# Optimization experiments

Hardware: AMD Instinct MI355X
Metric: run time of the kernel (lower is better)

The kernel has to match this reference:

```python
import jax, jax.numpy as jnp
import numpy as np

N_NODES = 20000
N_EDGES = 640000
IN_CH = 128
HID = 128
NUM_GRAPHS = 64


def setup_inputs() -> dict:
    key = jax.random.key(0)
    ks = jax.random.split(key, 16)
    s_in = 1.0 / np.sqrt(IN_CH)
    s_h = 1.0 / np.sqrt(HID)
    return {
        "x": jax.random.normal(ks[0], (N_NODES, IN_CH), jnp.float32),
        "edge_index": jax.random.randint(ks[1], (2, N_EDGES), 0, N_NODES, jnp.int64),
        "batch": jnp.sort(jax.random.randint(ks[2], (N_NODES,), 0, NUM_GRAPHS, jnp.int64)),
        "W1a": jax.random.normal(ks[3], (IN_CH, HID), jnp.float32) * s_in,
        "b1a": jnp.zeros((HID,), jnp.float32),
        "W1b": jax.random.normal(ks[4], (HID, HID), jnp.float32) * s_h,
        "b1b": jnp.zeros((HID,), jnp.float32),
        "W2a": jax.random.normal(ks[5], (HID, HID), jnp.float32) * s_h,
        "b2a": jnp.zeros((HID,), jnp.float32),
        "W2b": jax.random.normal(ks[6], (HID, HID), jnp.float32) * s_h,
        "b2b": jnp.zeros((HID,), jnp.float32),
        "fc_w": jax.random.normal(ks[7], (HID, 1), jnp.float32) * s_h,
        "fc_b": jnp.zeros((1,), jnp.float32),
    }


def _gin_conv(x, edge_index, Wa, ba, Wb, bb):
    # PyG GINConv (eps=0, sum aggregation): MLP(x + scatter_add(x[src] -> dst))
    src, dst = edge_index[0], edge_index[1]
    agg = jax.ops.segment_sum(x[src], dst, num_segments=x.shape[0])
    h = x + agg
    h = jax.nn.relu(h @ Wa + ba)
    return h @ Wb + bb


def reference(x, edge_index, batch, W1a, b1a, W1b, b1b, W2a, b2a, W2b, b2b, fc_w, fc_b):
    h = jax.nn.relu(_gin_conv(x, edge_index, W1a, b1a, W1b, b1b))
    # dropout: inference mode -> identity
    h = jax.nn.relu(_gin_conv(h, edge_index, W2a, b2a, W2b, b2b))
    # global_mean_pool over graph ids
    sums = jax.ops.segment_sum(h, batch, num_segments=NUM_GRAPHS)
    counts = jax.ops.segment_sum(jnp.ones((h.shape[0],), h.dtype), batch, num_segments=NUM_GRAPHS)
    pooled = sums / jnp.maximum(counts, 1.0)[:, None]
    return pooled @ fc_w + fc_b
```

## Files before the change

### kernel.cpp

```cpp
#include <hip/hip_runtime.h>

#define NN 20000
#define NE 640000
#define CH 128
#define NG 64
#define CAP 96
#define CSTR 16

typedef unsigned short u16;
typedef unsigned char u8;
typedef __attribute__((ext_vector_type(8))) short short8;
typedef __attribute__((ext_vector_type(4))) float floatx4;
typedef __attribute__((ext_vector_type(2))) float floatx2;

__device__ __forceinline__ u16 f2b(float f) {
    unsigned int u = __float_as_uint(f);
    u += 0x7fff + ((u >> 16) & 1);
    return (u16)(u >> 16);
}
__device__ __forceinline__ u8 f2q(float f) {
    return (u8)(__builtin_amdgcn_cvt_pk_fp8_f32(f, f, 0, false) & 0xff);
}
__device__ __forceinline__ void acc16(uint4 q, floatx2* a) {
    a[0] += __builtin_amdgcn_cvt_pk_f32_fp8(q.x, false);
    a[1] += __builtin_amdgcn_cvt_pk_f32_fp8(q.x, true);
    a[2] += __builtin_amdgcn_cvt_pk_f32_fp8(q.y, false);
    a[3] += __builtin_amdgcn_cvt_pk_f32_fp8(q.y, true);
    a[4] += __builtin_amdgcn_cvt_pk_f32_fp8(q.z, false);
    a[5] += __builtin_amdgcn_cvt_pk_f32_fp8(q.z, true);
    a[6] += __builtin_amdgcn_cvt_pk_f32_fp8(q.w, false);
    a[7] += __builtin_amdgcn_cvt_pk_f32_fp8(q.w, true);
}
__device__ __forceinline__ void round32(const u8* __restrict__ in, const int* __restrict__ ssrc,
                                        int base, int slot, int boff, floatx2* a) {
    int4 si = *(const int4*)&ssrc[base + slot * 4];
    uint4 q0 = *(const uint4*)(in + (size_t)si.x * CH + boff);
    uint4 q1 = *(const uint4*)(in + (size_t)si.y * CH + boff);
    uint4 q2 = *(const uint4*)(in + (size_t)si.z * CH + boff);
    uint4 q3 = *(const uint4*)(in + (size_t)si.w * CH + boff);
    acc16(q0, a); acc16(q1, a); acc16(q2, a); acc16(q3, a);
}
__device__ __forceinline__ void tail32(const u8* __restrict__ in, const int* __restrict__ ssrc,
                                       int base, int e, int slot, int boff, floatx2* a) {
    int i0 = base + slot * 4;
    int4 si = *(const int4*)&ssrc[i0];
    bool ok0 = i0 + 0 < e, ok1 = i0 + 1 < e, ok2 = i0 + 2 < e, ok3 = i0 + 3 < e;
    int s0 = ok0 ? si.x : 0, s1 = ok1 ? si.y : 0, s2 = ok2 ? si.z : 0, s3 = ok3 ? si.w : 0;
    uint4 q0 = *(const uint4*)(in + (size_t)s0 * CH + boff);
    uint4 q1 = *(const uint4*)(in + (size_t)s1 * CH + boff);
    uint4 q2 = *(const uint4*)(in + (size_t)s2 * CH + boff);
    uint4 q3 = *(const uint4*)(in + (size_t)s3 * CH + boff);
    if (!ok0) q0 = make_uint4(0, 0, 0, 0);
    if (!ok1) q1 = make_uint4(0, 0, 0, 0);
    if (!ok2) q2 = make_uint4(0, 0, 0, 0);
    if (!ok3) q3 = make_uint4(0, 0, 0, 0);
    acc16(q0, a); acc16(q1, a); acc16(q2, a); acc16(q3, a);
}

__global__ __launch_bounds__(256) void prep(const float* __restrict__ x, u8* __restrict__ xq,
                                            const float* __restrict__ W1a, const float* __restrict__ W1b,
                                            const float* __restrict__ W2a, const float* __restrict__ W2b,
                                            u16* __restrict__ wt, float* __restrict__ gsum,
                                            const int* __restrict__ ei,
                                            int* __restrict__ cnt, int* __restrict__ ssrc) {
    int b = blockIdx.x;
    if (b < 2500) {
        int idx = (b * 256 + threadIdx.x) * 4;
        float4 v = *(const float4*)(x + idx);
        int pk = __builtin_amdgcn_cvt_pk_fp8_f32(v.x, v.y, 0, false);
        pk = __builtin_amdgcn_cvt_pk_fp8_f32(v.z, v.w, pk, true);
        *(unsigned int*)(xq + idx) = (unsigned int)pk;
    } else if (b < 2756) {
        int wi = b - 2500;
        int m = wi >> 6;
        int r = (wi & 63) * 256 + threadIdx.x;
        int j = r & 7, l16 = (r >> 3) & 15, quad = (r >> 7) & 3;
        int kc = (r >> 9) & 3, ct = (r >> 11) & 7;
        int n = ct * 16 + l16, k = kc * 32 + quad * 8 + j;
        const float* W = (m == 0) ? W1a : (m == 1) ? W1b : (m == 2) ? W2a : W2b;
        wt[m * 16384 + r] = f2b(W[k * 128 + n]);
    } else if (b < 2788) {
        gsum[(b - 2756) * 256 + threadIdx.x] = 0.f;
    } else {
        int e = (b - 2788) * 256 + threadIdx.x;
        int dst = ei[NE + e];
        int src = ei[e];
        int pos = atomicAdd(&cnt[dst * CSTR], 1);
        if (pos < CAP) ssrc[dst * CAP + pos] = src;
    }
}

template <int DO_POOL>
__global__ __launch_bounds__(512) void layer(const u8* __restrict__ in,
                                             const int* __restrict__ cnt, const int* __restrict__ ssrc,
                                             const u16* __restrict__ wtA, const u16* __restrict__ wtB,
                                             const float* __restrict__ biasA, const float* __restrict__ biasB,
                                             u8* __restrict__ outq,
                                             const int* __restrict__ batch, float* __restrict__ gsum) {
    __shared__ u16 A[16 * 136];
    __shared__ u16 H[16 * 136];
    int t = threadIdx.x, wave = t >> 6, lane = t & 63;
    int quad = lane >> 4, l16 = lane & 15;
    int nb = blockIdx.x * 16;

    int gg[4], glo = 0, ghi = 0;
    if (DO_POOL) {
        glo = batch[nb]; ghi = batch[nb + 15];
        #pragma unroll
        for (int r = 0; r < 4; ++r)
            gg[r] = batch[nb + quad * 4 + r];
    }

    int slot = lane >> 3, cg = lane & 7;
    int boff = cg * 16;
    {
        int n0 = nb + 2 * wave;
        int n1 = n0 + 1;
        int deg0 = cnt[n0 * CSTR]; if (deg0 > CAP) deg0 = CAP;
        int deg1 = cnt[n1 * CSTR]; if (deg1 > CAP) deg1 = CAP;
        floatx2 a0[8], a1[8];
        #pragma unroll
        for (int j = 0; j < 8; ++j) { a0[j] = (floatx2)(0.f); a1[j] = (floatx2)(0.f); }
        if (slot == 0) {
            uint4 q0 = *(const uint4*)(in + (size_t)n0 * CH + boff);
            uint4 q1 = *(const uint4*)(in + (size_t)n1 * CH + boff);
            acc16(q0, a0); acc16(q1, a1);
        }
        int b0 = n0 * CAP, e0 = b0 + deg0;
        int b1 = n1 * CAP, e1 = b1 + deg1;
        while ((b0 + 32 <= e0) | (b1 + 32 <= e1)) {
            if (b0 + 32 <= e0) { round32(in, ssrc, b0, slot, boff, a0); b0 += 32; }
            if (b1 + 32 <= e1) { round32(in, ssrc, b1, slot, boff, a1); b1 += 32; }
        }
        if (b0 < e0) tail32(in, ssrc, b0, e0, slot, boff, a0);
        if (b1 < e1) tail32(in, ssrc, b1, e1, slot, boff, a1);

        float f0[16], f1[16];
        #pragma unroll
        for (int j = 0; j < 8; ++j) {
            f0[2 * j] = a0[j][0]; f0[2 * j + 1] = a0[j][1];
            f1[2 * j] = a1[j][0]; f1[2 * j + 1] = a1[j][1];
        }
        #pragma unroll
        for (int j = 0; j < 16; ++j) {
            f0[j] += __shfl_xor(f0[j], 8);
            f0[j] += __shfl_xor(f0[j], 16);
            f0[j] += __shfl_xor(f0[j], 32);
            f1[j] += __shfl_xor(f1[j], 8);
            f1[j] += __shfl_xor(f1[j], 16);
            f1[j] += __shfl_xor(f1[j], 32);
        }
        if (slot == 0) {
            short8 o0a, o0b, o1a, o1b;
            #pragma unroll
            for (int j = 0; j < 8; ++j) {
                o0a[j] = (short)f2b(f0[j]);     o0b[j] = (short)f2b(f0[8 + j]);
                o1a[j] = (short)f2b(f1[j]);     o1b[j] = (short)f2b(f1[8 + j]);
            }
            *(short8*)&A[(2 * wave) * 136 + boff] = o0a;
            *(short8*)&A[(2 * wave) * 136 + boff + 8] = o0b;
            *(short8*)&A[(2 * wave + 1) * 136 + boff] = o1a;
            *(short8*)&A[(2 * wave + 1) * 136 + boff + 8] = o1b;
        }
    }
    __syncthreads();

    short8 af[4];
    #pragma unroll
    for (int kc = 0; kc < 4; ++kc)
        af[kc] = *(const short8*)&A[l16 * 136 + kc * 32 + quad * 8];

    {
        int ct = wave;
        floatx4 a0 = (floatx4)(0.f);
        #pragma unroll
        for (int kc = 0; kc < 4; ++kc) {
            short8 bf = *(const short8*)(wtA + (((ct * 4 + kc) * 4 + quad) * 16 + l16) * 8);
            a0 = __builtin_amdgcn_mfma_f32_16x16x32_bf16(af[kc], bf, a0, 0, 0, 0);
        }
        float bv = biasA[ct * 16 + l16];
        #pragma unroll
        for (int r = 0; r < 4; ++r)
            H[(quad * 4 + r) * 136 + ct * 16 + l16] = f2b(fmaxf(a0[r] + bv, 0.f));
    }
    __syncthreads();

    short8 af2[4];
    #pragma unroll
    for (int kc = 0; kc < 4; ++kc)
        af2[kc] = *(const short8*)&H[l16 * 136 + kc * 32 + quad * 8];

    {
        int ct = wave;
        floatx4 a0 = (floatx4)(0.f);
        #pragma unroll
        for (int kc = 0; kc < 4; ++kc) {
            short8 bf = *(const short8*)(wtB + (((ct * 4 + kc) * 4 + quad) * 16 + l16) * 8);
            a0 = __builtin_amdgcn_mfma_f32_16x16x32_bf16(af2[kc], bf, a0, 0, 0, 0);
        }
        int col = ct * 16 + l16;
        float bv = biasB[col];
        if (DO_POOL) {
            float vr[4];
            #pragma unroll
            for (int r = 0; r < 4; ++r) vr[r] = fmaxf(a0[r] + bv, 0.f);
            for (int g = glo; g <= ghi; ++g) {
                float s = 0.f;
                #pragma unroll
                for (int r = 0; r < 4; ++r) s += (gg[r] == g) ? vr[r] : 0.f;
                s += __shfl_xor(s, 16);
                s += __shfl_xor(s, 32);
                if (lane < 16) atomicAdd(&gsum[g * CH + col], s);
            }
        } else {
            #pragma unroll
            for (int r = 0; r < 4; ++r) {
                int row = nb + quad * 4 + r;
                outq[(size_t)row * CH + col] = f2q(fmaxf(a0[r] + bv, 0.f));
            }
        }
    }
}

__global__ __launch_bounds__(128) void pool_final(const float* __restrict__ gsum, const int* __restrict__ batch,
                                                  const float* __restrict__ fcw, const float* __restrict__ fcb,
                                                  float* __restrict__ outp) {
    int g = blockIdx.x, t = threadIdx.x;
    __shared__ int se[2];
    if (t < 2) {
        int target = g + t, lo = 0, hi = NN;
        while (lo < hi) { int mid = (lo + hi) >> 1; if (batch[mid] < target) lo = mid + 1; else hi = mid; }
        se[t] = lo;
    }
    __syncthreads();
    int cnt = se[1] - se[0]; if (cnt < 1) cnt = 1;
    float v = gsum[g * CH + t] * fcw[t] / (float)cnt;
    __shared__ float red[128];
    red[t] = v; __syncthreads();
    for (int s = 64; s > 0; s >>= 1) { if (t < s) red[t] += red[t + s]; __syncthreads(); }
    if (t == 0) outp[g] = red[0] + fcb[0];
}

extern "C" void kernel_launch(void* const* d_in, const int* in_sizes, int n_in,
                              void* d_out, int out_size, void* d_ws, size_t ws_size,
                              hipStream_t stream) {
    const float* x   = (const float*)d_in[0];
    const int*   ei  = (const int*)d_in[1];
    const int* batch = (const int*)d_in[2];
    const float* W1a = (const float*)d_in[3];
    const float* b1a = (const float*)d_in[4];
    const float* W1b = (const float*)d_in[5];
    const float* b1b = (const float*)d_in[6];
    const float* W2a = (const float*)d_in[7];
    const float* b2a = (const float*)d_in[8];
    const float* W2b = (const float*)d_in[9];
    const float* b2b = (const float*)d_in[10];
    const float* fcw = (const float*)d_in[11];
    const float* fcb = (const float*)d_in[12];
    float* out = (float*)d_out;

    char* w = (char*)d_ws;
    u8*  xq   = (u8*)w;  w += (size_t)NN * CH;
    u8*  hq   = (u8*)w;  w += (size_t)NN * CH;
    u16* wt   = (u16*)w; w += (size_t)4 * 16384 * 2;
    int* cnt  = (int*)w; w += (size_t)NN * CSTR * 4;
    float* gsum = (float*)w; w += (size_t)NG * CH * 4;
    int* ssrc = (int*)w; w += (size_t)NN * CAP * 4;

    hipMemsetAsync(cnt, 0, (size_t)NN * CSTR * 4, stream);

    prep<<<5288, 256, 0, stream>>>(x, xq, W1a, W1b, W2a, W2b, wt, gsum, ei, cnt, ssrc);

    layer<0><<<1250, 512, 0, stream>>>(xq, cnt, ssrc, wt + 0 * 16384, wt + 1 * 16384, b1a, b1b, hq, batch, gsum);
    layer<1><<<1250, 512, 0, stream>>>(hq, cnt, ssrc, wt + 2 * 16384, wt + 3 * 16384, b2a, b2b, hq, batch, gsum);

    pool_final<<<NG, 128, 0, stream>>>(gsum, batch, fcw, fcb, out);
}
```

Measured before the change: 174.4 us.

## Process 32 nodes per block with four interleaved gathers per wave

Each layer block now handles 32 nodes instead of 16. Each wave interleaves the neighbor gathers of four nodes instead of two, and the MFMA stages run over two 16-row tiles, which halves the grid. The aim is more memory-level parallelism per wave and weight-fragment loads amortised over more rows. The cost is higher register pressure from four accumulator sets, and only 625 blocks to fill the GPU, which may hurt occupancy and load balance.

Result: slower. 196.3 us (+12.6%).

```diff
diff --git a/kernel.cpp b/kernel.cpp
--- a/kernel.cpp
+++ b/kernel.cpp
@@ -55,6 +55,24 @@
     if (!ok2) q2 = make_uint4(0, 0, 0, 0);
     if (!ok3) q3 = make_uint4(0, 0, 0, 0);
     acc16(q0, a); acc16(q1, a); acc16(q2, a); acc16(q3, a);
+}
+__device__ __forceinline__ void reduce_store(floatx2* a, u16* Arow, int slot, int boff) {
+    float f[16];
+    #pragma unroll
+    for (int j = 0; j < 8; ++j) { f[2 * j] = a[j][0]; f[2 * j + 1] = a[j][1]; }
+    #pragma unroll
+    for (int j = 0; j < 16; ++j) {
+        f[j] += __shfl_xor(f[j], 8);
+        f[j] += __shfl_xor(f[j], 16);
+        f[j] += __shfl_xor(f[j], 32);
+    }
+    if (slot == 0) {
+        short8 oa, ob;
+        #pragma unroll
+        for (int j = 0; j < 8; ++j) { oa[j] = (short)f2b(f[j]); ob[j] = (short)f2b(f[8 + j]); }
+        *(short8*)&Arow[boff] = oa;
+        *(short8*)&Arow[boff + 8] = ob;
+    }
 }
 
 __global__ __launch_bounds__(256) void prep(const float* __restrict__ x, u8* __restrict__ xq,
@@ -97,81 +115,62 @@
                                              const float* __restrict__ biasA, const float* __restrict__ biasB,
                                              u8* __restrict__ outq,
                                              const int* __restrict__ batch, float* __restrict__ gsum) {
-    __shared__ u16 A[16 * 136];
-    __shared__ u16 H[16 * 136];
+    __shared__ u16 A[32 * 136];
+    __shared__ u16 H[32 * 136];
     int t = threadIdx.x, wave = t >> 6, lane = t & 63;
     int quad = lane >> 4, l16 = lane & 15;
-    int nb = blockIdx.x * 16;
-
-    int gg[4], glo = 0, ghi = 0;
-    if (DO_POOL) {
-        glo = batch[nb]; ghi = batch[nb + 15];
-        #pragma unroll
-        for (int r = 0; r < 4; ++r)
-            gg[r] = batch[nb + quad * 4 + r];
-    }
+    int nb = blockIdx.x * 32;
 
     int slot = lane >> 3, cg = lane & 7;
     int boff = cg * 16;
     {
-        int n0 = nb + 2 * wave;
-        int n1 = n0 + 1;
+        int n0 = nb + 4 * wave, n1 = n0 + 1, n2 = n0 + 2, n3 = n0 + 3;
         int deg0 = cnt[n0 * CSTR]; if (deg0 > CAP) deg0 = CAP;
         int deg1 = cnt[n1 * CSTR]; if (deg1 > CAP) deg1 = CAP;
-        floatx2 a0[8], a1[8];
-        #pragma unroll
-        for (int j = 0; j < 8; ++j) { a0[j] = (floatx2)(0.f); a1[j] = (floatx2)(0.f); }
+        int deg2 = cnt[n2 * CSTR]; if (deg2 > CAP) deg2 = CAP;
+        int deg3 = cnt[n3 * CSTR]; if (deg3 > CAP) deg3 = CAP;
+        floatx2 a0[8], a1[8], a2[8], a3[8];
+        #pragma unroll
+        for (int j = 0; j < 8; ++j) {
+            a0[j] = (floatx2)(0.f); a1[j] = (floatx2)(0.f);
+            a2[j] = (floatx2)(0.f); a3[j] = (floatx2)(0.f);
+        }
         if (slot == 0) {
             uint4 q0 = *(const uint4*)(in + (size_t)n0 * CH + boff);
             uint4 q1 = *(const uint4*)(in + (size_t)n1 * CH + boff);
-            acc16(q0, a0); acc16(q1, a1);
+            uint4 q2 = *(const uint4*)(in + (size_t)n2 * CH + boff);
+            uint4 q3 = *(const uint4*)(in + (size_t)n3 * CH + boff);
+            acc16(q0, a0); acc16(q1, a1); acc16(q2, a2); acc16(q3, a3);
         }
         int b0 = n0 * CAP, e0 = b0 + deg0;
         int b1 = n1 * CAP, e1 = b1 + deg1;
-        while ((b0 + 32 <= e0) | (b1 + 32 <= e1)) {
+        int b2 = n2 * CAP, e2 = b2 + deg2;
+        int b3 = n3 * CAP, e3 = b3 + deg3;
+        while ((b0 + 32 <= e0) | (b1 + 32 <= e1) | (b2 + 32 <= e2) | (b3 + 32 <= e3)) {
             if (b0 + 32 <= e0) { round32(in, ssrc, b0, slot, boff, a0); b0 += 32; }
             if (b1 + 32 <= e1) { round32(in, ssrc, b1, slot, boff, a1); b1 += 32; }
+            if (b2 + 32 <= e2) { round32(in, ssrc, b2, slot, boff, a2); b2 += 32; }
+            if (b3 + 32 <= e3) { round32(in, ssrc, b3, slot, boff, a3); b3 += 32; }
         }
         if (b0 < e0) tail32(in, ssrc, b0, e0, slot, boff, a0);
         if (b1 < e1) tail32(in, ssrc, b1, e1, slot, boff, a1);
-
-        float f0[16], f1[16];
-        #pragma unroll
-        for (int j = 0; j < 8; ++j) {
-            f0[2 * j] = a0[j][0]; f0[2 * j + 1] = a0[j][1];
-            f1[2 * j] = a1[j][0]; f1[2 * j + 1] = a1[j][1];
-        }
-        #pragma unroll
-        for (int j = 0; j < 16; ++j) {
-            f0[j] += __shfl_xor(f0[j], 8);
-            f0[j] += __shfl_xor(f0[j], 16);
-            f0[j] += __shfl_xor(f0[j], 32);
-            f1[j] += __shfl_xor(f1[j], 8);
-            f1[j] += __shfl_xor(f1[j], 16);
-            f1[j] += __shfl_xor(f1[j], 32);
-        }
-        if (slot == 0) {
-            short8 o0a, o0b, o1a, o1b;
-            #pragma unroll
-            for (int j = 0; j < 8; ++j) {
-                o0a[j] = (short)f2b(f0[j]);     o0b[j] = (short)f2b(f0[8 + j]);
-                o1a[j] = (short)f2b(f1[j]);     o1b[j] = (short)f2b(f1[8 + j]);
-            }
-            *(short8*)&A[(2 * wave) * 136 + boff] = o0a;
-            *(short8*)&A[(2 * wave) * 136 + boff + 8] = o0b;
-            *(short8*)&A[(2 * wave + 1) * 136 + boff] = o1a;
-            *(short8*)&A[(2 * wave + 1) * 136 + boff + 8] = o1b;
-        }
+        if (b2 < e2) tail32(in, ssrc, b2, e2, slot, boff, a2);
+        if (b3 < e3) tail32(in, ssrc, b3, e3, slot, boff, a3);
+
+        reduce_store(a0, &A[(4 * wave + 0) * 136], slot, boff);
+        reduce_store(a1, &A[(4 * wave + 1) * 136], slot, boff);
+        reduce_store(a2, &A[(4 * wave + 2) * 136], slot, boff);
+        reduce_store(a3, &A[(4 * wave + 3) * 136], slot, boff);
     }
     __syncthreads();
 
-    short8 af[4];
-    #pragma unroll
-    for (int kc = 0; kc < 4; ++kc)
-        af[kc] = *(const short8*)&A[l16 * 136 + kc * 32 + quad * 8];
-
-    {
-        int ct = wave;
+    int ct = wave;
+    #pragma unroll
+    for (int rt = 0; rt < 2; ++rt) {
+        short8 af[4];
+        #pragma unroll
+        for (int kc = 0; kc < 4; ++kc)
+            af[kc] = *(const short8*)&A[(rt * 16 + l16) * 136 + kc * 32 + quad * 8];
         floatx4 a0 = (floatx4)(0.f);
         #pragma unroll
         for (int kc = 0; kc < 4; ++kc) {
@@ -181,17 +180,16 @@
         float bv = biasA[ct * 16 + l16];
         #pragma unroll
         for (int r = 0; r < 4; ++r)
-            H[(quad * 4 + r) * 136 + ct * 16 + l16] = f2b(fmaxf(a0[r] + bv, 0.f));
+            H[(rt * 16 + quad * 4 + r) * 136 + ct * 16 + l16] = f2b(fmaxf(a0[r] + bv, 0.f));
     }
     __syncthreads();
 
-    short8 af2[4];
-    #pragma unroll
-    for (int kc = 0; kc < 4; ++kc)
-        af2[kc] = *(const short8*)&H[l16 * 136 + kc * 32 + quad * 8];
-
-    {
-        int ct = wave;
+    #pragma unroll
+    for (int rt = 0; rt < 2; ++rt) {
+        short8 af2[4];
+        #pragma unroll
+        for (int kc = 0; kc < 4; ++kc)
+            af2[kc] = *(const short8*)&H[(rt * 16 + l16) * 136 + kc * 32 + quad * 8];
         floatx4 a0 = (floatx4)(0.f);
         #pragma unroll
         for (int kc = 0; kc < 4; ++kc) {
@@ -201,6 +199,11 @@
         int col = ct * 16 + l16;
         float bv = biasB[col];
         if (DO_POOL) {
+            int rbase = nb + rt * 16;
+            int glo = batch[rbase], ghi = batch[rbase + 15];
+            int gg[4];
+            #pragma unroll
+            for (int r = 0; r < 4; ++r) gg[r] = batch[rbase + quad * 4 + r];
             float vr[4];
             #pragma unroll
             for (int r = 0; r < 4; ++r) vr[r] = fmaxf(a0[r] + bv, 0.f);
@@ -215,7 +218,7 @@
         } else {
             #pragma unroll
             for (int r = 0; r < 4; ++r) {
-                int row = nb + quad * 4 + r;
+                int row = nb + rt * 16 + quad * 4 + r;
                 outq[(size_t)row * CH + col] = f2q(fmaxf(a0[r] + bv, 0.f));
             }
         }
@@ -271,8 +274,8 @@
 
     prep<<<5288, 256, 0, stream>>>(x, xq, W1a, W1b, W2a, W2b, wt, gsum, ei, cnt, ssrc);
 
-    layer<0><<<1250, 512, 0, stream>>>(xq, cnt, ssrc, wt + 0 * 16384, wt + 1 * 16384, b1a, b1b, hq, batch, gsum);
-    layer<1><<<1250, 512, 0, stream>>>(hq, cnt, ssrc, wt + 2 * 16384, wt + 3 * 16384, b2a, b2b, hq, batch, gsum);
+    layer<0><<<625, 512, 0, stream>>>(xq, cnt, ssrc, wt + 0 * 16384, wt + 1 * 16384, b1a, b1b, hq, batch, gsum);
+    layer<1><<<625, 512, 0, stream>>>(hq, cnt, ssrc, wt + 2 * 16384, wt + 3 * 16384, b2a, b2b, hq, batch, gsum);
 
     pool_final<<<NG, 128, 0, stream>>>(gsum, batch, fcw, fcb, out);
 }
```

## Store neighbor lists as u16 position-major and use 8-wide tail rounds

Applied to the files above, without the earlier changes.

Neighbor source ids are stored as 16-bit values in a position-major array (pos*NN+dst) instead of 32-bit node-major slots. This halves index memory traffic and footprint. The gather loop now handles leftovers in 8-edge rounds plus a predicated tail, instead of one masked 32-edge round that issued wasted loads. The trade-off is that index loads become scalar strided reads rather than one vector load per lane-slot.

Measured after the change: 170.5 us. -2.2%, faster.

```diff
diff --git a/kernel.cpp b/kernel.cpp
--- a/kernel.cpp
+++ b/kernel.cpp
@@ -31,30 +31,50 @@
     a[6] += __builtin_amdgcn_cvt_pk_f32_fp8(q.w, false);
     a[7] += __builtin_amdgcn_cvt_pk_f32_fp8(q.w, true);
 }
-__device__ __forceinline__ void round32(const u8* __restrict__ in, const int* __restrict__ ssrc,
-                                        int base, int slot, int boff, floatx2* a) {
-    int4 si = *(const int4*)&ssrc[base + slot * 4];
-    uint4 q0 = *(const uint4*)(in + (size_t)si.x * CH + boff);
-    uint4 q1 = *(const uint4*)(in + (size_t)si.y * CH + boff);
-    uint4 q2 = *(const uint4*)(in + (size_t)si.z * CH + boff);
-    uint4 q3 = *(const uint4*)(in + (size_t)si.w * CH + boff);
-    acc16(q0, a); acc16(q1, a); acc16(q2, a); acc16(q3, a);
-}
-__device__ __forceinline__ void tail32(const u8* __restrict__ in, const int* __restrict__ ssrc,
-                                       int base, int e, int slot, int boff, floatx2* a) {
-    int i0 = base + slot * 4;
-    int4 si = *(const int4*)&ssrc[i0];
-    bool ok0 = i0 + 0 < e, ok1 = i0 + 1 < e, ok2 = i0 + 2 < e, ok3 = i0 + 3 < e;
-    int s0 = ok0 ? si.x : 0, s1 = ok1 ? si.y : 0, s2 = ok2 ? si.z : 0, s3 = ok3 ? si.w : 0;
+__device__ __forceinline__ void round32P(const u8* __restrict__ in, const u16* __restrict__ ssrc,
+                                         int n, int r8, int slot, int boff, floatx2* a) {
+    int s0 = ssrc[(r8 + 0 + slot) * NN + n];
+    int s1 = ssrc[(r8 + 8 + slot) * NN + n];
+    int s2 = ssrc[(r8 + 16 + slot) * NN + n];
+    int s3 = ssrc[(r8 + 24 + slot) * NN + n];
     uint4 q0 = *(const uint4*)(in + (size_t)s0 * CH + boff);
     uint4 q1 = *(const uint4*)(in + (size_t)s1 * CH + boff);
     uint4 q2 = *(const uint4*)(in + (size_t)s2 * CH + boff);
     uint4 q3 = *(const uint4*)(in + (size_t)s3 * CH + boff);
-    if (!ok0) q0 = make_uint4(0, 0, 0, 0);
-    if (!ok1) q1 = make_uint4(0, 0, 0, 0);
-    if (!ok2) q2 = make_uint4(0, 0, 0, 0);
-    if (!ok3) q3 = make_uint4(0, 0, 0, 0);
     acc16(q0, a); acc16(q1, a); acc16(q2, a); acc16(q3, a);
+}
+__device__ __forceinline__ void round8P(const u8* __restrict__ in, const u16* __restrict__ ssrc,
+                                        int n, int r8, int slot, int boff, floatx2* a) {
+    int src = ssrc[(r8 + slot) * NN + n];
+    uint4 q = *(const uint4*)(in + (size_t)src * CH + boff);
+    acc16(q, a);
+}
+__device__ __forceinline__ void tail8P(const u8* __restrict__ in, const u16* __restrict__ ssrc,
+                                       int n, int r8, int deg, int slot, int boff, floatx2* a) {
+    int p = r8 + slot;
+    if (p < deg) {
+        int src = ssrc[p * NN + n];
+        uint4 q = *(const uint4*)(in + (size_t)src * CH + boff);
+        acc16(q, a);
+    }
+}
+__device__ __forceinline__ void reduce_store(floatx2* a, u16* Arow, int slot, int boff) {
+    float f[16];
+    #pragma unroll
+    for (int j = 0; j < 8; ++j) { f[2 * j] = a[j][0]; f[2 * j + 1] = a[j][1]; }
+    #pragma unroll
+    for (int j = 0; j < 16; ++j) {
+        f[j] += __shfl_xor(f[j], 8);
+        f[j] += __shfl_xor(f[j], 16);
+        f[j] += __shfl_xor(f[j], 32);
+    }
+    if (slot == 0) {
+        short8 oa, ob;
+        #pragma unroll
+        for (int j = 0; j < 8; ++j) { oa[j] = (short)f2b(f[j]); ob[j] = (short)f2b(f[8 + j]); }
+        *(short8*)&Arow[boff] = oa;
+        *(short8*)&Arow[boff + 8] = ob;
+    }
 }
 
 __global__ __launch_bounds__(256) void prep(const float* __restrict__ x, u8* __restrict__ xq,
@@ -62,7 +82,7 @@
                                             const float* __restrict__ W2a, const float* __restrict__ W2b,
                                             u16* __restrict__ wt, float* __restrict__ gsum,
                                             const int* __restrict__ ei,
-                                            int* __restrict__ cnt, int* __restrict__ ssrc) {
+                                            int* __restrict__ cnt, u16* __restrict__ ssrc) {
     int b = blockIdx.x;
     if (b < 2500) {
         int idx = (b * 256 + threadIdx.x) * 4;
@@ -86,13 +106,13 @@
         int dst = ei[NE + e];
         int src = ei[e];
         int pos = atomicAdd(&cnt[dst * CSTR], 1);
-        if (pos < CAP) ssrc[dst * CAP + pos] = src;
+        if (pos < CAP) ssrc[pos * NN + dst] = (u16)src;
     }
 }
 
 template <int DO_POOL>
 __global__ __launch_bounds__(512) void layer(const u8* __restrict__ in,
-                                             const int* __restrict__ cnt, const int* __restrict__ ssrc,
+                                             const int* __restrict__ cnt, const u16* __restrict__ ssrc,
                                              const u16* __restrict__ wtA, const u16* __restrict__ wtB,
                                              const float* __restrict__ biasA, const float* __restrict__ biasB,
                                              u8* __restrict__ outq,
@@ -126,42 +146,20 @@
             uint4 q1 = *(const uint4*)(in + (size_t)n1 * CH + boff);
             acc16(q0, a0); acc16(q1, a1);
         }
-        int b0 = n0 * CAP, e0 = b0 + deg0;
-        int b1 = n1 * CAP, e1 = b1 + deg1;
-        while ((b0 + 32 <= e0) | (b1 + 32 <= e1)) {
-            if (b0 + 32 <= e0) { round32(in, ssrc, b0, slot, boff, a0); b0 += 32; }
-            if (b1 + 32 <= e1) { round32(in, ssrc, b1, slot, boff, a1); b1 += 32; }
-        }
-        if (b0 < e0) tail32(in, ssrc, b0, e0, slot, boff, a0);
-        if (b1 < e1) tail32(in, ssrc, b1, e1, slot, boff, a1);
-
-        float f0[16], f1[16];
-        #pragma unroll
-        for (int j = 0; j < 8; ++j) {
-            f0[2 * j] = a0[j][0]; f0[2 * j + 1] = a0[j][1];
-            f1[2 * j] = a1[j][0]; f1[2 * j + 1] = a1[j][1];
-        }
-        #pragma unroll
-        for (int j = 0; j < 16; ++j) {
-            f0[j] += __shfl_xor(f0[j], 8);
-            f0[j] += __shfl_xor(f0[j], 16);
-            f0[j] += __shfl_xor(f0[j], 32);
-            f1[j] += __shfl_xor(f1[j], 8);
-            f1[j] += __shfl_xor(f1[j], 16);
-            f1[j] += __shfl_xor(f1[j], 32);
-        }
-        if (slot == 0) {
-            short8 o0a, o0b, o1a, o1b;
-            #pragma unroll
-            for (int j = 0; j < 8; ++j) {
-                o0a[j] = (short)f2b(f0[j]);     o0b[j] = (short)f2b(f0[8 + j]);
-                o1a[j] = (short)f2b(f1[j]);     o1b[j] = (short)f2b(f1[8 + j]);
-            }
-            *(short8*)&A[(2 * wave) * 136 + boff] = o0a;
-            *(short8*)&A[(2 * wave) * 136 + boff + 8] = o0b;
-            *(short8*)&A[(2 * wave + 1) * 136 + boff] = o1a;
-            *(short8*)&A[(2 * wave + 1) * 136 + boff + 8] = o1b;
-        }
+        int r0 = 0, r1 = 0;
+        while ((r0 + 32 <= deg0) | (r1 + 32 <= deg1)) {
+            if (r0 + 32 <= deg0) { round32P(in, ssrc, n0, r0, slot, boff, a0); r0 += 32; }
+            if (r1 + 32 <= deg1) { round32P(in, ssrc, n1, r1, slot, boff, a1); r1 += 32; }
+        }
+        while ((r0 + 8 <= deg0) | (r1 + 8 <= deg1)) {
+            if (r0 + 8 <= deg0) { round8P(in, ssrc, n0, r0, slot, boff, a0); r0 += 8; }
+            if (r1 + 8 <= deg1) { round8P(in, ssrc, n1, r1, slot, boff, a1); r1 += 8; }
+        }
+        if (r0 < deg0) tail8P(in, ssrc, n0, r0, deg0, slot, boff, a0);
+        if (r1 < deg1) tail8P(in, ssrc, n1, r1, deg1, slot, boff, a1);
+
+        reduce_store(a0, &A[(2 * wave) * 136], slot, boff);
+        reduce_store(a1, &A[(2 * wave + 1) * 136], slot, boff);
     }
     __syncthreads();
 
@@ -265,7 +263,7 @@
     u16* wt   = (u16*)w; w += (size_t)4 * 16384 * 2;
     int* cnt  = (int*)w; w += (size_t)NN * CSTR * 4;
     float* gsum = (float*)w; w += (size_t)NG * CH * 4;
-    int* ssrc = (int*)w; w += (size_t)NN * CAP * 4;
+    u16* ssrc = (u16*)w; w += (size_t)CAP * NN * 2;
 
     hipMemsetAsync(cnt, 0, (size_t)NN * CSTR * 4, stream);
 
```
